# Kernel tuning notes

Measured on AMD Instinct MI355X. Metric: run time of the kernel, lower is better.

Reference implementation:

```python
import jax, jax.numpy as jnp
import numpy as np

F_, V, ED = 16, 1000, 16
B = 65536
D_IN = F_ * ED            # 256
STAR = [256, 512, 256]    # star layers
FCN = [256, 128, 64]      # mmoe expert layers
DOM, TSK, EXP = 3, 2, 8
KDT = DOM * TSK           # 6 gates/towers
SKIP_WEIGHT = 0.5
EPS = 1e-5


def layernorm(x, g, b):
    mu = jnp.mean(x, -1, keepdims=True)
    var = jnp.mean((x - mu) ** 2, -1, keepdims=True)
    return (x - mu) * jax.lax.rsqrt(var + EPS) * g + b


def mlp1(x, W, b, g, be):
    # Linear -> LayerNorm -> ReLU (MLP_N with one block)
    return jax.nn.relu(layernorm(x @ W + b, g, be))


def stack2(h, W1, b1, g1, be1, W2, b2, g2, be2):
    # vectorized bank of 2-block MLP_N experts; h: [B,D0], W1: [E,D0,D1]
    h1 = jax.nn.relu(layernorm(jnp.einsum('bd,edh->ebh', h, W1) + b1[:, None, :], g1[:, None, :], be1[:, None, :]))
    h2 = jax.nn.relu(layernorm(jnp.einsum('ebd,edh->ebh', h1, W2) + b2[:, None, :], g2[:, None, :], be2[:, None, :]))
    return h2  # [E,B,H]


def setup_inputs() -> dict:
    key = jax.random.key(0)
    ks = iter(jax.random.split(key, 64))

    def nrm(shape, scale=0.05):
        return jax.random.normal(next(ks), shape, jnp.float32) * scale

    inp = {}
    inp['x'] = jax.random.randint(next(ks), (F_, B), 0, 3).astype(jnp.int32)
    inp['emb_tables'] = nrm((F_, V, ED))
    inp['skip_W'] = nrm((D_IN, STAR[2])); inp['skip_b'] = jnp.zeros((STAR[2],))
    inp['skip_g'] = jnp.ones((STAR[2],)); inp['skip_be'] = jnp.zeros((STAR[2],))
    inp['shared_W'] = nrm((STAR[0], STAR[1])); inp['shared_b'] = jnp.zeros((STAR[1],))
    inp['slot_W'] = nrm((DOM, STAR[0], STAR[1])); inp['slot_b'] = jnp.zeros((DOM, STAR[1]))
    inp['star_W'] = nrm((STAR[1], STAR[2])); inp['star_b'] = jnp.zeros((STAR[2],))
    inp['star_g'] = jnp.ones((STAR[2],)); inp['star_be'] = jnp.zeros((STAR[2],))
    inp['dskip_W'] = nrm((KDT, STAR[2], FCN[-1])); inp['dskip_b'] = jnp.zeros((KDT, FCN[-1]))
    inp['dskip_g'] = jnp.ones((KDT, FCN[-1])); inp['dskip_be'] = jnp.zeros((KDT, FCN[-1]))
    for pre, n in (('exp', EXP), ('dexp', DOM), ('texp', TSK)):
        inp[pre + '_W1'] = nrm((n, FCN[0], FCN[1])); inp[pre + '_b1'] = jnp.zeros((n, FCN[1]))
        inp[pre + '_g1'] = jnp.ones((n, FCN[1])); inp[pre + '_be1'] = jnp.zeros((n, FCN[1]))
        inp[pre + '_W2'] = nrm((n, FCN[1], FCN[2])); inp[pre + '_b2'] = jnp.zeros((n, FCN[2]))
        inp[pre + '_g2'] = jnp.ones((n, FCN[2])); inp[pre + '_be2'] = jnp.zeros((n, FCN[2]))
    inp['gate_W'] = nrm((KDT, FCN[0], EXP)); inp['gate_b'] = jnp.zeros((KDT, EXP))
    inp['tow_W1'] = nrm((KDT, FCN[-1], FCN[-1])); inp['tow_b1'] = jnp.zeros((KDT, FCN[-1]))
    inp['tow_g'] = jnp.ones((KDT, FCN[-1])); inp['tow_be'] = jnp.zeros((KDT, FCN[-1]))
    inp['tow_W2'] = nrm((KDT, FCN[-1])); inp['tow_b2'] = jnp.zeros((KDT,))
    return inp


def _forward(x, emb_tables, skip_W, skip_b, skip_g, skip_be, shared_W, shared_b,
             slot_W, slot_b, star_W, star_b, star_g, star_be,
             dskip_W, dskip_b, dskip_g, dskip_be,
             exp_W1, exp_b1, exp_g1, exp_be1, exp_W2, exp_b2, exp_g2, exp_be2,
             dexp_W1, dexp_b1, dexp_g1, dexp_be1, dexp_W2, dexp_b2, dexp_g2, dexp_be2,
             texp_W1, texp_b1, texp_g1, texp_be1, texp_W2, texp_b2, texp_g2, texp_be2,
             gate_W, gate_b, tow_W1, tow_b1, tow_g, tow_be, tow_W2, tow_b2):
    domain_id = x[-1]                                          # [B] in {0,1,2}
    embs = jax.vmap(lambda t, i: t[i])(emb_tables, x)          # [F,B,ED]
    input_emb = jnp.moveaxis(embs, 0, 1).reshape(x.shape[1], D_IN)  # [B,256]

    skip = mlp1(input_emb, skip_W, skip_b, skip_g, skip_be)    # [B,256]

    # STAR: per-domain elementwise-product weights, domain masked select
    slot_out = jnp.einsum('bd,kdh->kbh', input_emb, slot_W * shared_W[None]) + slot_b[:, None, :] + shared_b  # [D,B,512]
    onehot = (domain_id[None, :] == jnp.arange(DOM)[:, None]).astype(slot_out.dtype)  # [D,B]
    emb0 = jnp.sum(onehot[:, :, None] * slot_out, axis=0)      # [B,512]
    emb = mlp1(emb0, star_W, star_b, star_g, star_be) + skip   # [B,256]

    # gates use emb.detach()
    gate = jax.nn.softmax(jnp.einsum('bd,kde->kbe', jax.lax.stop_gradient(emb), gate_W) + gate_b[:, None, :], axis=-1)  # [6,B,8]

    fea = stack2(emb, exp_W1, exp_b1, exp_g1, exp_be1, exp_W2, exp_b2, exp_g2, exp_be2)        # [8,B,64]
    dfea = stack2(emb, dexp_W1, dexp_b1, dexp_g1, dexp_be1, dexp_W2, dexp_b2, dexp_g2, dexp_be2)  # [3,B,64]
    tfea = stack2(emb, texp_W1, texp_b1, texp_g1, texp_be1, texp_W2, texp_b2, texp_g2, texp_be2)  # [2,B,64]
    dskip = jax.nn.relu(layernorm(jnp.einsum('bd,kdh->kbh', emb, dskip_W) + dskip_b[:, None, :], dskip_g[:, None, :], dskip_be[:, None, :]))  # [6,B,64]

    d_idx = jnp.arange(KDT) % DOM
    t_idx = jnp.arange(KDT) % TSK
    fused = jnp.einsum('kbe,ebh->kbh', gate, fea) + dfea[d_idx] + tfea[t_idx] + SKIP_WEIGHT * dskip  # [6,B,64]

    h = jax.nn.relu(layernorm(jnp.einsum('kbh,khj->kbj', fused, tow_W1) + tow_b1[:, None, :], tow_g[:, None, :], tow_be[:, None, :]))
    probs = jax.nn.sigmoid(jnp.einsum('kbh,kh->kb', h, tow_W2) + tow_b2[:, None])  # [6,B]

    # output[:, i] with i = t*DOM + d -> [B,T,D]; pick per-sample domain column
    out = jnp.moveaxis(probs, 0, 1).reshape(-1, TSK, DOM)
    result = jnp.take_along_axis(out, domain_id[:, None, None].astype(jnp.int32), axis=2)[:, :, 0]  # [B,T]
    return result


def reference(x, emb_tables, skip_W, skip_b, skip_g, skip_be, shared_W, shared_b,
              slot_W, slot_b, star_W, star_b, star_g, star_be,
              dskip_W, dskip_b, dskip_g, dskip_be,
              exp_W1, exp_b1, exp_g1, exp_be1, exp_W2, exp_b2, exp_g2, exp_be2,
              dexp_W1, dexp_b1, dexp_g1, dexp_be1, dexp_W2, dexp_b2, dexp_g2, dexp_be2,
              texp_W1, texp_b1, texp_g1, texp_be1, texp_W2, texp_b2, texp_g2, texp_be2,
              gate_W, gate_b, tow_W1, tow_b1, tow_g, tow_be, tow_W2, tow_b2):
    return _forward(x, emb_tables, skip_W, skip_b, skip_g, skip_be, shared_W, shared_b,
                    slot_W, slot_b, star_W, star_b, star_g, star_be,
                    dskip_W, dskip_b, dskip_g, dskip_be,
                    exp_W1, exp_b1, exp_g1, exp_be1, exp_W2, exp_b2, exp_g2, exp_be2,
                    dexp_W1, dexp_b1, dexp_g1, dexp_be1, dexp_W2, dexp_b2, dexp_g2, dexp_be2,
                    texp_W1, texp_b1, texp_g1, texp_be1, texp_W2, texp_b2, texp_g2, texp_be2,
                    gate_W, gate_b, tow_W1, tow_b1, tow_g, tow_be, tow_W2, tow_b2)
```

## Files before the change

kernel.cpp:

```cpp
#include <hip/hip_runtime.h>
#include <stdint.h>

#define B_TOT 65536

typedef __attribute__((ext_vector_type(8))) short s16x8;
typedef __attribute__((ext_vector_type(4))) float f32x4;
typedef unsigned short u16;
typedef unsigned int u32;
typedef unsigned long long u64;

#define OFF_SKIPW   0
#define OFF_MD      65536
#define OFF_GATEW   262144
#define OFF_EXPW1   274432
#define OFF_EXPW2   700416
#define OFF_DSKIPW  806912
#define OFF_TOWW1   905216
#define OFF_BVEC    929792
#define OFF_PAR     931328
#define OFF_PARF    941568
#define OFF_EMB     944640
#define OFF_PERM    17852928
#define OFF_CNT     17985024

// ... 26 lines not shown
}

template<int NT>
__device__ __forceinline__ void ln16(const f32x4* a, float invN, float* mu, float* rs){
  float s[4], q[4];
#pragma unroll
  for(int r=0;r<4;r++){ float aa=0.f,bb=0.f;
#pragma unroll
    for(int t=0;t<NT;t++){ float v=a[t][r]; aa+=v; bb+=v*v; }
    s[r]=aa; q[r]=bb; }
#pragma unroll
  for(int m=1;m<16;m<<=1){
#pragma unroll
    for(int r=0;r<4;r++){ s[r]+=__shfl_xor(s[r],m,16); q[r]+=__shfl_xor(q[r],m,16); } }
#pragma unroll
  for(int r=0;r<4;r++){ float m_=s[r]*invN; float v=q[r]*invN-m_*m_; mu[r]=m_; rs[r]=rsqrtf(v+1e-5f); }
}

__global__ __launch_bounds__(64) void k_sortinit(u16* __restrict__ ws){
  if(threadIdx.x<8) ((u32*)(ws+OFF_CNT))[threadIdx.x]=0u;
}
__global__ __launch_bounds__(256) void k_count(const int* __restrict__ x, u16* __restrict__ ws){
  u32* cnt=(u32*)(ws+OFF_CNT);
  int i=blockIdx.x*256+threadIdx.x;
  int lane=threadIdx.x&63;
  int d=x[15*B_TOT+i];
  u64 m0=__ballot(d==0), m1=__ballot(d==1), m2=__ballot(d==2);
  if(lane==0){
    if(m0) atomicAdd(&cnt[0],(u32)__popcll(m0));
    if(m1) atomicAdd(&cnt[1],(u32)__popcll(m1));
    if(m2) atomicAdd(&cnt[2],(u32)__popcll(m2));
  }
}
__global__ __launch_bounds__(256) void k_scatter(const int* __restrict__ x, u16* __restrict__ ws){
  u32* cnt=(u32*)(ws+OFF_CNT);
  u32* perm=(u32*)(ws+OFF_PERM);
  int i=blockIdx.x*256+threadIdx.x;
  int lane=threadIdx.x&63;
  int d=x[15*B_TOT+i];
  u32 c0=cnt[0], c1=cnt[1];
  u32 s1=c0, s2=c0+c1;
  u64 m0=__ballot(d==0), m1=__ballot(d==1), m2=__ballot(d==2);
  u32 b0v=0,b1v=0,b2v=0;
  if(lane==0){
    if(m0) b0v=atomicAdd(&cnt[3],(u32)__popcll(m0));
    if(m1) b1v=atomicAdd(&cnt[4],(u32)__popcll(m1));
    if(m2) b2v=atomicAdd(&cnt[5],(u32)__popcll(m2));
  }
  b0v=__shfl(b0v,0,64); b1v=__shfl(b1v,0,64); b2v=__shfl(b2v,0,64);
  u64 below=(1ull<<lane)-1ull;
  u32 pos;
  if(d==0)      pos=    b0v+(u32)__popcll(m0&below);
  else if(d==1) pos=s1+ b1v+(u32)__popcll(m1&below);
  else          pos=s2+ b2v+(u32)__popcll(m2&below);
  perm[pos]=(u32)i;
}

__global__ __launch_bounds__(256) void k_pack(
    const float* __restrict__ skip_W, const float* __restrict__ gate_W,
    const float* __restrict__ exp_W1, const float* __restrict__ dexp_W1, const float* __restrict__ texp_W1,
    const float* __restrict__ exp_W2, const float* __restrict__ dexp_W2, const float* __restrict__ texp_W2,
    const float* __restrict__ dskip_W, const float* __restrict__ tow_W1,
    u16* __restrict__ ws)
{
  int i=blockIdx.x*256+threadIdx.x;
  if(i>=OFF_BVEC) return;
  if(i>=OFF_MD && i<OFF_GATEW) return;
  float v;
  if(i<OFF_MD){
    int l=i; int j=l&7, lane=(l>>3)&63, kt=(l>>9)&7, ct=l>>12;
    int n=ct*16+(lane&15), k=kt*32+((lane>>4)<<3)+j;
    v = skip_W[k*256+n];
  } else if(i<OFF_EXPW1){
    int l=i-OFF_GATEW; int j=l&7, lane=(l>>3)&63, kt=(l>>9)&7, ct=l>>12;
    int n=ct*16+(lane&15), k=kt*32+((lane>>4)<<3)+j;
    int k6=n>>3, e=n&7;
    v = gate_W[(k6*256+k)*8+e];
  } else if(i<OFF_EXPW2){
    int l=i-OFF_EXPW1; int e=l>>15, r=l&32767;
    int j=r&7, lane=(r>>3)&63, kt=(r>>9)&7, ct=r>>12;
    int n=ct*16+(lane&15), k=kt*32+((lane>>4)<<3)+j;
    v = (e<8)? exp_W1[(e*256+k)*128+n] : (e<11)? dexp_W1[((e-8)*256+k)*128+n] : texp_W1[((e-11)*256+k)*128+n];
  } else if(i<OFF_DSKIPW){
    int l=i-OFF_EXPW2; int e=l>>13, r=l&8191;
    int j=r&7, lane=(r>>3)&63, kt=(r>>9)&3, ct=r>>11;
    int n=ct*16+(lane&15), k=kt*32+((lane>>4)<<3)+j;
    v = (e<8)? exp_W2[(e*128+k)*64+n] : (e<11)? dexp_W2[((e-8)*128+k)*64+n] : texp_W2[((e-11)*128+k)*64+n];
  } else if(i<OFF_TOWW1){
    int l=i-OFF_DSKIPW; int s=l>>14, r=l&16383;
    int j=r&7, lane=(r>>3)&63, kt=(r>>9)&7, ct=r>>12;
    int n=ct*16+(lane&15), k=kt*32+((lane>>4)<<3)+j;
    v = dskip_W[(s*256+k)*64+n];
  } else {
    int l=i-OFF_TOWW1; int s=l>>12, r=l&4095;
    int j=r&7, lane=(r>>3)&63, kt=(r>>9)&1, ct=r>>10;
    int n=ct*16+(lane&15), k=kt*32+((lane>>4)<<3)+j;
    v = tow_W1[(s*64+k)*64+n];
  }
  ws[i]=f2bf(v);
}

__global__ __launch_bounds__(256) void k_packpar(
    const float* __restrict__ exp_b1,const float* __restrict__ exp_g1,const float* __restrict__ exp_be1,
    const float* __restrict__ exp_b2,const float* __restrict__ exp_g2,const float* __restrict__ exp_be2,
    const float* __restrict__ dexp_b1,const float* __restrict__ dexp_g1,const float* __restrict__ dexp_be1,
    const float* __restrict__ dexp_b2,const float* __restrict__ dexp_g2,const float* __restrict__ dexp_be2,
    const float* __restrict__ texp_b1,const float* __restrict__ texp_g1,const float* __restrict__ texp_be1,
    const float* __restrict__ texp_b2,const float* __restrict__ texp_g2,const float* __restrict__ texp_be2,
    const float* __restrict__ dskip_b,const float* __restrict__ dskip_g,const float* __restrict__ dskip_be,
    const float* __restrict__ gate_b,
    const float* __restrict__ tow_b1,const float* __restrict__ tow_g,const float* __restrict__ tow_be,
    const float* __restrict__ tow_W2,const float* __restrict__ tow_b2,
    const float* __restrict__ skip_b,const float* __restrict__ skip_g,const float* __restrict__ skip_be,
    const float* __restrict__ star_b,const float* __restrict__ star_g,const float* __restrict__ star_be,
    u16* __restrict__ ws)
{
  int i=blockIdx.x*256+threadIdx.x;
  float* parf=(float*)(ws+OFF_PARF);
  if(i<10240){
    float v=0.f;
    if(i<PAR_DSK){
      int e=i/576, r=i%576;
      const float *b1,*g1,*be1,*b2,*g2,*be2;
      if(e<8){ b1=exp_b1+e*128; g1=exp_g1+e*128; be1=exp_be1+e*128;
               b2=exp_b2+e*64;  g2=exp_g2+e*64;  be2=exp_be2+e*64; }
      else if(e<11){ int q=e-8; b1=dexp_b1+q*128; g1=dexp_g1+q*128; be1=dexp_be1+q*128;
               b2=dexp_b2+q*64; g2=dexp_g2+q*64; be2=dexp_be2+q*64; }
      else { int q=e-11; b1=texp_b1+q*128; g1=texp_g1+q*128; be1=texp_be1+q*128;
               b2=texp_b2+q*64; g2=texp_g2+q*64; be2=texp_be2+q*64; }
      v = (r<128)? b1[r] : (r<256)? g1[r-128] : (r<384)? be1[r-256]
        : (r<448)? b2[r-384] : (r<512)? g2[r-448] : be2[r-512];
    } else if(i<PAR_TOW){
      int l=i-PAR_DSK; int j=l/192, r=l%192;
      v = (r<64)? dskip_b[j*64+r] : (r<128)? dskip_g[j*64+r-64] : dskip_be[j*64+r-128];
    } else if(i<PAR_GB){
      int l=i-PAR_TOW; int k6=l/256, r=l%256;
      v = (r<64)? tow_b1[k6*64+r] : (r<128)? tow_g[k6*64+r-64]
        : (r<192)? tow_be[k6*64+r-128] : tow_W2[k6*64+r-192];
    } else if(i<PAR_TB2){ v=gate_b[i-PAR_GB]; }
    else if(i<PAR_TB2+6){ v=tow_b2[i-PAR_TB2]; }
    ws[OFF_PAR+i]=f2bf(v);
  } else if(i<10240+1536){
    int l=i-10240;
    parf[l] = (l<256)? skip_b[l] : (l<512)? skip_g[l-256] : (l<768)? skip_be[l-512]
            : (l<1024)? star_b[l-768] : (l<1280)? star_g[l-1024] : star_be[l-1280];
  }
}

__global__ __launch_bounds__(256) void k_fold(
    const float* __restrict__ slot_W, const float* __restrict__ shared_W, const float* __restrict__ star_W,
    const float* __restrict__ slot_b, const float* __restrict__ shared_b,
    u16* __restrict__ ws)
{
  __shared__ float w[512];
  int bid=blockIdx.x, tid=threadIdx.x;
  if(bid<768){
    int d=bid>>8, k=bid&255;
    for(int j=tid;j<512;j+=256) w[j]=slot_W[(d*256+k)*512+j]*shared_W[k*512+j];
    __syncthreads();
    int n=tid; float a=0.f;
    for(int j=0;j<512;j++) a += w[j]*star_W[j*256+n];
    int ct=n>>4, l15=n&15, kt=k>>5, hi=(k>>3)&3, j8=k&7;
    ws[OFF_MD + d*65536 + (((ct*8+kt)*64 + hi*16 + l15)<<3) + j8] = f2bf(a);
  } else {
    int d=bid-768;
    for(int j=tid;j<512;j+=256) w[j]=slot_b[d*512+j]+shared_b[j];
    __syncthreads();
// ... 88 lines not shown
      for(int r=0;r<4;r++){
        float v=fmaxf((acc[rt][ct][r]-mu[r])*rs[r]*gv+bev,0.f);
        trbw[(rt*16+hq*4+r)*264 + col]=f2bf(v);
      }
    }
  }
  lds_fence();
#pragma unroll
  for(int rt=0;rt<2;rt++){
    int rtg=(b0>>4)+wv*2+rt;
#pragma unroll
    for(int kt=0;kt<8;kt++){
      s16x8 v=*(const s16x8*)(trbw + (rt*16+l15)*264 + kt*32+hq*8);
      *(s16x8*)(embp + (((size_t)(rtg*8+kt)*64+lane)<<3)) = v;
    }
  }
  __syncthreads();
  gstage(wsu+OFF_MD+dlo*65536, Wb[0], 16384, wv, lane, 4);
  __syncthreads();
  cur=0;

#pragma unroll
  for(int rt=0;rt<2;rt++)
#pragma unroll
    for(int ct=0;ct<16;ct++) acc[rt][ct]=fz;
  for(int dd=dlo;dd<=dhi;dd++){
#pragma unroll
    for(int c=0;c<8;c++){
      if(c<7)        gstage(wsu+OFF_MD+dd*65536+(c+1)*8192, Wb[cur^1], 16384, wv, lane, 4);
      else if(dd<dhi) gstage(wsu+OFF_MD+(dd+1)*65536,       Wb[cur^1], 16384, wv, lane, 4);
      const u16* B=Wb[cur];
#pragma unroll
      for(int kt=0;kt<8;kt++){
        s16x8 a0=(dmA[0]==dd)?af[0][kt]:zf;
        s16x8 a1=(dmA[1]==dd)?af[1][kt]:zf;
#pragma unroll
        for(int i=0;i<2;i++){
          s16x8 bf=*(const s16x8*)(B + (((i*8+kt)*64+lane)<<3));
          acc[0][c*2+i]=mfma16(a0,bf,acc[0][c*2+i]);
          acc[1][c*2+i]=mfma16(a1,bf,acc[1][c*2+i]);
        }
      }
      __syncthreads(); cur^=1;
    }
  }

#pragma unroll
  for(int rt=0;rt<2;rt++){
#pragma unroll
    for(int ct=0;ct<16;ct++){
      int col=ct*16+l15; float sb=parF[768+col];
#pragma unroll
      for(int r=0;r<4;r++) acc[rt][ct][r] += sb + bvecL[dm[rt][r]*256+col];
    }
    float mu[4],rs[4];
    ln16<16>(&acc[rt][0], 1.f/256.f, mu, rs);
#pragma unroll
    for(int ct=0;ct<16;ct++){
      int col=ct*16+l15;
      float gv=parF[1024+col], bev=parF[1280+col];
#pragma unroll
      for(int r=0;r<4;r++){
        float v=fmaxf((acc[rt][ct][r]-mu[r])*rs[r]*gv+bev,0.f);
        trbw[(rt*16+hq*4+r)*264 + col]=f2bf(v);
      }
    }
  }
  lds_fence();
#pragma unroll
  for(int rt=0;rt<2;rt++){
    int rtg=(b0>>4)+wv*2+rt;
#pragma unroll
    for(int kt=0;kt<8;kt++){
      s16x8 vs=*(const s16x8*)(trbw + (rt*16+l15)*264 + kt*32+hq*8);
      s16x8 vk=*(const s16x8*)(embp + (((size_t)(rtg*8+kt)*64+lane)<<3));
      union{ u16 h[8]; s16x8 v; } t;
#pragma unroll
      for(int j=0;j<8;j++) t.h[j]=f2bf(bf2f((u16)vs[j])+bf2f((u16)vk[j]));
      *(s16x8*)(embp + (((size_t)(rtg*8+kt)*64+lane)<<3)) = t.v;
    }
  }
}

__device__ __forceinline__ void glds1k(const u16* g, u16* l, int lane){
  __builtin_amdgcn_global_load_lds(
    (const __attribute__((address_space(1))) u32*)((const char*)g + lane*16),
    (__attribute__((address_space(3))) u32*)((char*)l), 16,0,0);
}
__device__ __forceinline__ void stage16k4(const u16* g, u16* l, int wv, int lane){
#pragma unroll
  for(int q=0;q<4;q++) glds1k(g + wv*2048 + q*512, l + wv*2048 + q*512, lane);
}
__device__ __forceinline__ void stage8k4(const u16* g, u16* l, int wv, int lane){
#pragma unroll
  for(int q=0;q<2;q++) glds1k(g + wv*1024 + q*512, l + wv*1024 + q*512, lane);
}
__device__ __forceinline__ void stage_phase4(int p, int dlo, int ndom,
    const u16* wsu, u16* slot, int wv, int lane){
  const int NU=10+ndom;
  const int P1=2+5*NU, P2=P1+4*ndom;
  if(p<2){ stage16k4(wsu+OFF_GATEW+p*8192, slot, wv, lane); return; }
  if(p<P1){ int q=p-2, ui=q/5, s=q%5;
    int u = (ui<8)? ui : (ui<8+ndom)? (8+dlo+(ui-8)) : (11+(ui-8-ndom));
    const u16* g = (s<4)? (wsu+OFF_EXPW1+u*32768+s*8192) : (wsu+OFF_EXPW2+u*8192);
    stage16k4(g, slot, wv, lane); return; }
  if(p<P2){ int q=p-P1; int dd=dlo+(q>>2); int j=(q&2)?(3+dd):dd; int half=q&1;
    stage16k4(wsu+OFF_DSKIPW+j*16384+half*8192, slot, wv, lane); return; }
  { int dd=dlo+(p-P2);
    stage8k4(wsu+OFF_TOWW1+dd*4096,     slot,      wv, lane);
    stage8k4(wsu+OFF_TOWW1+(3+dd)*4096, slot+4096, wv, lane); }
}
__device__ __forceinline__ void endph(){
  asm volatile("s_waitcnt vmcnt(0) lgkmcnt(0)\n\ts_barrier" ::: "memory");
  __builtin_amdgcn_sched_barrier(0);
}

__global__ __launch_bounds__(256,2) void k_B(
    const int* __restrict__ x, u16* __restrict__ wsu, float* __restrict__ out)
{
  __shared__ __align__(16) u16 Wb[2][8192];
  __shared__ __align__(16) u16 trb[4][32][136];
  __shared__ __align__(16) u32 gateF[128][8];
  __shared__ __align__(16) u16 parT[4096];

  const int tid=threadIdx.x, lane=tid&63, wv=tid>>6;
  const int l15=lane&15, hq=lane>>4;
  const int b0=blockIdx.x*128, rowbase=b0+wv*32;
  const f32x4 fz={0.f,0.f,0.f,0.f};
  const u16* embp=wsu+OFF_EMB;
  const u16* parE=wsu+OFF_PAR;
  const u32* perm=(const u32*)(wsu+OFF_PERM);
  u16* trbw=&trb[wv][0][0];

  const int dlo=__builtin_amdgcn_readfirstlane(x[15*B_TOT+(int)perm[b0]]);
  const int dhi=__builtin_amdgcn_readfirstlane(x[15*B_TOT+(int)perm[b0+127]]);
  const int ndom=dhi-dlo+1;
  const int NU=10+ndom;
  const int P1=2+5*NU, P2=P1+4*ndom, P3=P2+ndom;

  stage_phase4(0, dlo, ndom, wsu, &Wb[0][0], wv, lane);
  stage8k4(wsu+OFF_PAR+PAR_DSK, parT, wv, lane);

  u32 pv[2][4]; int dm[2][4];
#pragma unroll
  for(int rt=0;rt<2;rt++)
#pragma unroll
    for(int r=0;r<4;r++){
      u32 pp=perm[rowbase + rt*16 + hq*4 + r];
      pv[rt][r]=pp;
      dm[rt][r]=x[15*B_TOT+(int)pp];
    }

  s16x8 af[2][8];
#pragma unroll
  for(int rt=0;rt<2;rt++){
    int rtg=(rowbase>>4)+rt;
#pragma unroll
    for(int kt=0;kt<8;kt++)
      af[rt][kt]=*(const s16x8*)(embp + (((size_t)(rtg*8+kt)*64+lane)<<3));
  }

  f32x4 fa0[2][4], fa1[2][4];
#pragma unroll
  for(int rt=0;rt<2;rt++)
#pragma unroll
    for(int ct=0;ct<4;ct++){ fa0[rt][ct]=fz; fa1[rt][ct]=fz; }

  asm volatile("s_waitcnt vmcnt(0)" ::: "memory");
  __syncthreads();
  int p=0;

  {
    f32x4 gacc[2][3];
#pragma unroll
    for(int rt=0;rt<2;rt++)
#pragma unroll
      for(int ct=0;ct<3;ct++) gacc[rt][ct]=fz;
    stage_phase4(1, dlo, ndom, wsu, &Wb[1][0], wv, lane);
#pragma unroll
    for(int kt=0;kt<8;kt++)
#pragma unroll
      for(int i=0;i<2;i++){
        s16x8 bf=*(const s16x8*)(&Wb[0][0] + (((i*8+kt)*64+lane)<<3));
        gacc[0][i]=mfma16(af[0][kt],bf,gacc[0][i]);
        gacc[1][i]=mfma16(af[1][kt],bf,gacc[1][i]);
      }
    endph(); p=1;

    stage_phase4(2, dlo, ndom, wsu, &Wb[0][0], wv, lane);
#pragma unroll
    for(int kt=0;kt<8;kt++){
      s16x8 bf=*(const s16x8*)(&Wb[1][0] + ((kt*64+lane)<<3));
      gacc[0][2]=mfma16(af[0][kt],bf,gacc[0][2]);
      gacc[1][2]=mfma16(af[1][kt],bf,gacc[1][2]);
    }
    u16* gFh=(u16*)&gateF[0][0];
#pragma unroll
    for(int rt=0;rt<2;rt++)
#pragma unroll
      for(int ct=0;ct<3;ct++){
        int k6=ct*2+(l15>>3), e=l15&7;
        float gb=bf2f(parT[(PAR_GB-PAR_DSK) + k6*8+e]);
#pragma unroll
        for(int r=0;r<4;r++){
          float v=gacc[rt][ct][r]+gb;
          float mx=v;
          mx=fmaxf(mx,__shfl_xor(mx,1,8)); mx=fmaxf(mx,__shfl_xor(mx,2,8)); mx=fmaxf(mx,__shfl_xor(mx,4,8));
          float pe=__expf(v-mx);
          float ss=pe;
          ss+=__shfl_xor(ss,1,8); ss+=__shfl_xor(ss,2,8); ss+=__shfl_xor(ss,4,8);
          int brow=wv*32+rt*16+hq*4+r;
          int dmv=dm[rt][r];
          if(k6==dmv)   gFh[(brow*8+e)*2]  =f2bf(pe/ss);
          if(k6==3+dmv) gFh[(brow*8+e)*2+1]=f2bf(pe/ss);
        }
      }
    lds_fence();
    endph(); p=2;
  }

  for(int ui=0;ui<NU;ui++){
    const int u = (ui<8)? ui : (ui<8+ndom)? (8+dlo+(ui-8)) : (11+(ui-8-ndom));
    f32x4 acc1[2][8];
#pragma unroll
    for(int rt=0;rt<2;rt++)
#pragma unroll
      for(int ct=0;ct<8;ct++) acc1[rt][ct]=fz;
    for(int c=0;c<4;c++){
      const u16* Bw=&Wb[p&1][0];
      if(p+1<P3) stage_phase4(p+1, dlo, ndom, wsu, &Wb[(p+1)&1][0], wv, lane);
#pragma unroll
      for(int kt=0;kt<8;kt++)
#pragma unroll
        for(int i=0;i<2;i++){
          s16x8 bf=*(const s16x8*)(Bw + (((i*8+kt)*64+lane)<<3));
          acc1[0][c*2+i]=mfma16(af[0][kt],bf,acc1[0][c*2+i]);
          acc1[1][c*2+i]=mfma16(af[1][kt],bf,acc1[1][c*2+i]);
        }
      endph(); p++;
    }
    {
      const u16* Bw=&Wb[p&1][0];
      if(p+1<P3) stage_phase4(p+1, dlo, ndom, wsu, &Wb[(p+1)&1][0], wv, lane);
      const u16* pe_=parE + u*576;
#pragma unroll
      for(int rt=0;rt<2;rt++){
#pragma unroll
        for(int ct=0;ct<8;ct++){ float bb=bf2f(pe_[ct*16+l15]);
#pragma unroll
          for(int r=0;r<4;r++) acc1[rt][ct][r]+=bb; }
        float mu[4],rs[4],nm[4];
        ln16<8>(&acc1[rt][0],1.f/128.f,mu,rs);
#pragma unroll
        for(int r=0;r<4;r++) nm[r]=-mu[r]*rs[r];
#pragma unroll
        for(int ct=0;ct<8;ct++){
          int col=ct*16+l15;
          float gv=bf2f(pe_[128+col]), bev=bf2f(pe_[256+col]);
#pragma unroll
          for(int r=0;r<4;r++){
            float vn=fmaf(acc1[rt][ct][r],rs[r],nm[r]);
            trbw[(rt*16+hq*4+r)*136+col]=f2bf(fmaxf(fmaf(vn,gv,bev),0.f));
          }
        }
      }
      lds_fence();
      s16x8 af2[2][4];
#pragma unroll
      for(int rt=0;rt<2;rt++)
#pragma unroll
        for(int kt=0;kt<4;kt++)
          af2[rt][kt]=*(const s16x8*)(trbw+(rt*16+l15)*136+kt*32+hq*8);
      f32x4 acc2[2][4];
#pragma unroll
      for(int rt=0;rt<2;rt++)
#pragma unroll
        for(int ct=0;ct<4;ct++) acc2[rt][ct]=fz;
#pragma unroll
      for(int kt=0;kt<4;kt++)
#pragma unroll
        for(int ct=0;ct<4;ct++){
          s16x8 bf=*(const s16x8*)(Bw + (((ct*4+kt)*64+lane)<<3));
          acc2[0][ct]=mfma16(af2[0][kt],bf,acc2[0][ct]);
          acc2[1][ct]=mfma16(af2[1][kt],bf,acc2[1][ct]);
        }
#pragma unroll
      for(int rt=0;rt<2;rt++){
#pragma unroll
        for(int ct=0;ct<4;ct++){ float bb=bf2f(pe_[384+ct*16+l15]);
#pragma unroll
          for(int r=0;r<4;r++) acc2[rt][ct][r]+=bb; }
        float mu[4],rs[4],nm[4];
        ln16<4>(&acc2[rt][0],1.f/64.f,mu,rs);
#pragma unroll
        for(int r=0;r<4;r++) nm[r]=-mu[r]*rs[r];
        float g0v[4],g1v[4];
        if(ui<8){
#pragma unroll
          for(int r=0;r<4;r++){ u32 gg=gateF[wv*32+rt*16+hq*4+r][ui];
            g0v[r]=bf2f((u16)(gg&0xffffu)); g1v[r]=bf2f((u16)(gg>>16)); }
        } else if(ui<8+ndom){
          int du=dlo+(ui-8);
#pragma unroll
          for(int r=0;r<4;r++){ float m=(dm[rt][r]==du)?1.f:0.f; g0v[r]=m; g1v[r]=m; }
        } else {
          int q=ui-8-ndom;
#pragma unroll
          for(int r=0;r<4;r++){
            g0v[r]=((dm[rt][r]&1)==q)?1.f:0.f;
            g1v[r]=(((dm[rt][r]+1)&1)==q)?1.f:0.f;
          }
        }
#pragma unroll
        for(int ct=0;ct<4;ct++){
          int col=ct*16+l15;
          float gv=bf2f(pe_[448+col]), bev=bf2f(pe_[512+col]);
#pragma unroll
          for(int r=0;r<4;r++){
            float vn=fmaf(acc2[rt][ct][r],rs[r],nm[r]);
            float o=fmaxf(fmaf(vn,gv,bev),0.f);
            fa0[rt][ct][r]=fmaf(g0v[r],o,fa0[rt][ct][r]);
            fa1[rt][ct][r]=fmaf(g1v[r],o,fa1[rt][ct][r]);
          }
        }
      }
      endph(); p++;
    }
  }

  for(int dq=0;dq<2*ndom;dq++){
    const int dd=dlo+(dq>>1);
    const int jj=(dq&1)? (3+dd) : dd;
    f32x4 a3[2][4];
#pragma unroll
    for(int rt=0;rt<2;rt++)
#pragma unroll
      for(int ct=0;ct<4;ct++) a3[rt][ct]=fz;
    for(int c=0;c<2;c++){
      const u16* Bw=&Wb[p&1][0];
      if(p+1<P3) stage_phase4(p+1, dlo, ndom, wsu, &Wb[(p+1)&1][0], wv, lane);
#pragma unroll
      for(int kt=0;kt<8;kt++)
#pragma unroll
        for(int i=0;i<2;i++){
          s16x8 bf=*(const s16x8*)(Bw + (((i*8+kt)*64+lane)<<3));
          a3[0][c*2+i]=mfma16(af[0][kt],bf,a3[0][c*2+i]);
          a3[1][c*2+i]=mfma16(af[1][kt],bf,a3[1][c*2+i]);
        }
      if(c==1){
        const int pb=jj*192;
#pragma unroll
        for(int rt=0;rt<2;rt++){
#pragma unroll
          for(int ct=0;ct<4;ct++){ float bb=bf2f(parT[pb+ct*16+l15]);
#pragma unroll
            for(int r=0;r<4;r++) a3[rt][ct][r]+=bb; }
          float mu[4],rs[4],nm[4],mk[4];
          ln16<4>(&a3[rt][0],1.f/64.f,mu,rs);
#pragma unroll
          for(int r=0;r<4;r++){ nm[r]=-mu[r]*rs[r]; mk[r]=(dm[rt][r]==dd)?0.5f:0.f; }
#pragma unroll
          for(int ct=0;ct<4;ct++){
            int col=ct*16+l15;
            float gv=bf2f(parT[pb+64+col]), bev=bf2f(parT[pb+128+col]);
#pragma unroll
            for(int r=0;r<4;r++){
              float vn=fmaf(a3[rt][ct][r],rs[r],nm[r]);
              float o=fmaxf(fmaf(vn,gv,bev),0.f);
              if((dq&1)==0) fa0[rt][ct][r]=fmaf(mk[r],o,fa0[rt][ct][r]);
              else          fa1[rt][ct][r]=fmaf(mk[r],o,fa1[rt][ct][r]);
            }
          }
        }
      }
      endph(); p++;
    }
  }

#pragma unroll
  for(int rt=0;rt<2;rt++)
#pragma unroll
    for(int ct=0;ct<4;ct++)
#pragma unroll
      for(int r=0;r<4;r++){
        int rr=(rt*16+hq*4+r)*136 + ct*16+l15;
        trbw[rr]   =f2bf(fa0[rt][ct][r]);
        trbw[rr+64]=f2bf(fa1[rt][ct][r]);
      }
  lds_fence();
  s16x8 aft0[2][2], aft1[2][2];
#pragma unroll
  for(int rt=0;rt<2;rt++)
#pragma unroll
    for(int kt=0;kt<2;kt++){
      aft0[rt][kt]=*(const s16x8*)(trbw+(rt*16+l15)*136+kt*32+hq*8);
      aft1[rt][kt]=*(const s16x8*)(trbw+(rt*16+l15)*136+64+kt*32+hq*8);
    }

  for(int t=0;t<ndom;t++){
    const u16* Bw=&Wb[p&1][0];
    if(p+1<P3) stage_phase4(p+1, dlo, ndom, wsu, &Wb[(p+1)&1][0], wv, lane);
    const int dd=dlo+t;
#pragma unroll
    for(int s=0;s<2;s++){
      const int k6 = s? (3+dd) : dd;
      f32x4 ta[2][4];
#pragma unroll
      for(int rt=0;rt<2;rt++)
#pragma unroll
        for(int ct=0;ct<4;ct++) ta[rt][ct]=fz;
#pragma unroll
      for(int kt=0;kt<2;kt++)
#pragma unroll
        for(int ct=0;ct<4;ct++){
          s16x8 bf=*(const s16x8*)(Bw + s*4096 + (((ct*2+kt)*64+lane)<<3));
          if(s==0){ ta[0][ct]=mfma16(aft0[0][kt],bf,ta[0][ct]); ta[1][ct]=mfma16(aft0[1][kt],bf,ta[1][ct]); }
          else    { ta[0][ct]=mfma16(aft1[0][kt],bf,ta[0][ct]); ta[1][ct]=mfma16(aft1[1][kt],bf,ta[1][ct]); }
        }
      const int pb=(PAR_TOW-PAR_DSK)+k6*256;
#pragma unroll
      for(int rt=0;rt<2;rt++){
#pragma unroll
        for(int ct=0;ct<4;ct++){ float bb=bf2f(parT[pb+ct*16+l15]);
#pragma unroll
          for(int r=0;r<4;r++) ta[rt][ct][r]+=bb; }
        float mu[4],rs[4],nm[4];
        ln16<4>(&ta[rt][0],1.f/64.f,mu,rs);
#pragma unroll
        for(int r=0;r<4;r++) nm[r]=-mu[r]*rs[r];
        float pr[4]={0.f,0.f,0.f,0.f};
#pragma unroll
        for(int ct=0;ct<4;ct++){
          int col=ct*16+l15;
          float gv=bf2f(parT[pb+64+col]), bev=bf2f(parT[pb+128+col]), w2=bf2f(parT[pb+192+col]);
#pragma unroll
          for(int r=0;r<4;r++){
            float vn=fmaf(ta[rt][ct][r],rs[r],nm[r]);
            float o=fmaxf(fmaf(vn,gv,bev),0.f);
            pr[r]=fmaf(o,w2,pr[r]);
          }
        }
#pragma unroll
        for(int m=1;m<16;m<<=1){
#pragma unroll
          for(int r=0;r<4;r++) pr[r]+=__shfl_xor(pr[r],m,16);
        }
        if(l15==0){
          float tb2=bf2f(parT[(PAR_TB2-PAR_DSK)+k6]);
#pragma unroll
          for(int r=0;r<4;r++){
            if(dm[rt][r]==dd){
              float sv=pr[r]+tb2;
              out[(size_t)pv[rt][r]*2 + s] = 1.f/(1.f+__expf(-sv));
            }
          }
        }
      }
    }
    if(p+1<P3) endph();
    p++;
  }
}

extern "C" void kernel_launch(void* const* d_in, const int* in_sizes, int n_in,
                              void* d_out, int out_size, void* d_ws, size_t ws_size,
                              hipStream_t stream)
{
  if(ws_size < (size_t)(OFF_CNT+32)*2) return;

  const int*   x          =(const int*)  d_in[0];
  const float* emb_tables =(const float*)d_in[1];
  const float* skip_W     =(const float*)d_in[2];
  const float* skip_b     =(const float*)d_in[3];
  const float* skip_g     =(const float*)d_in[4];
  const float* skip_be    =(const float*)d_in[5];
  const float* shared_W   =(const float*)d_in[6];
  const float* shared_b   =(const float*)d_in[7];
  const float* slot_W     =(const float*)d_in[8];
  const float* slot_b     =(const float*)d_in[9];
  const float* star_W     =(const float*)d_in[10];
  const float* star_b     =(const float*)d_in[11];
  const float* star_g     =(const float*)d_in[12];
  const float* star_be    =(const float*)d_in[13];
  const float* dskip_W    =(const float*)d_in[14];
  const float* dskip_b    =(const float*)d_in[15];
  const float* dskip_g    =(const float*)d_in[16];
  const float* dskip_be   =(const float*)d_in[17];
  const float* exp_W1     =(const float*)d_in[18];
  const float* exp_b1     =(const float*)d_in[19];
  const float* exp_g1     =(const float*)d_in[20];
  const float* exp_be1    =(const float*)d_in[21];
  const float* exp_W2     =(const float*)d_in[22];
  const float* exp_b2     =(const float*)d_in[23];
  const float* exp_g2     =(const float*)d_in[24];
  const float* exp_be2    =(const float*)d_in[25];
  const float* dexp_W1    =(const float*)d_in[26];
  const float* dexp_b1    =(const float*)d_in[27];
  const float* dexp_g1    =(const float*)d_in[28];
  const float* dexp_be1   =(const float*)d_in[29];
  const float* dexp_W2    =(const float*)d_in[30];
  const float* dexp_b2    =(const float*)d_in[31];
  const float* dexp_g2    =(const float*)d_in[32];
  const float* dexp_be2   =(const float*)d_in[33];
  const float* texp_W1    =(const float*)d_in[34];
  const float* texp_b1    =(const float*)d_in[35];
  const float* texp_g1    =(const float*)d_in[36];
  const float* texp_be1   =(const float*)d_in[37];
  const float* texp_W2    =(const float*)d_in[38];
  const float* texp_b2    =(const float*)d_in[39];
  const float* texp_g2    =(const float*)d_in[40];
  const float* texp_be2   =(const float*)d_in[41];
  const float* gate_W     =(const float*)d_in[42];
  const float* gate_b     =(const float*)d_in[43];
  const float* tow_W1     =(const float*)d_in[44];
  const float* tow_b1     =(const float*)d_in[45];
  const float* tow_g      =(const float*)d_in[46];
  const float* tow_be     =(const float*)d_in[47];
  const float* tow_W2     =(const float*)d_in[48];
  const float* tow_b2     =(const float*)d_in[49];

  u16* wsu=(u16*)d_ws;
  float* out=(float*)d_out;

  k_sortinit<<<1,64,0,stream>>>(wsu);
  k_count<<<B_TOT/256,256,0,stream>>>(x,wsu);
  k_scatter<<<B_TOT/256,256,0,stream>>>(x,wsu);
  k_pack<<<(OFF_BVEC+255)/256,256,0,stream>>>(skip_W,gate_W,
      exp_W1,dexp_W1,texp_W1,exp_W2,dexp_W2,texp_W2,dskip_W,tow_W1,wsu);
  k_packpar<<<46,256,0,stream>>>(
      exp_b1,exp_g1,exp_be1,exp_b2,exp_g2,exp_be2,
      dexp_b1,dexp_g1,dexp_be1,dexp_b2,dexp_g2,dexp_be2,
      texp_b1,texp_g1,texp_be1,texp_b2,texp_g2,texp_be2,
      dskip_b,dskip_g,dskip_be,gate_b,
      tow_b1,tow_g,tow_be,tow_W2,tow_b2,
      skip_b,skip_g,skip_be,star_b,star_g,star_be,wsu);
  k_fold<<<771,256,0,stream>>>(slot_W,shared_W,star_W,slot_b,shared_b,wsu);
  k_front<<<B_TOT/128,256,0,stream>>>(x,emb_tables,wsu);
  k_B<<<B_TOT/128,256,0,stream>>>(x,wsu,out);
}
```

Baseline: 402.9 us.

## Load expert weights directly from global memory, drop LDS double-buffered staging

Removes the block-wide double-buffered global_load_lds weight staging and per-phase barriers. Each wave now reads MFMA B-fragments straight from global memory (through cache) and reads parameters from global instead of an LDS copy. Domain range is computed per wave rather than per block, and gate scratch becomes per-wave, so all block barriers disappear. Launch bounds drop to one block per SM, and a stray redundant assignment is added in the pack kernel. The aim is to remove barrier stalls and LDS traffic, at the cost of more global/L2 loads per wave and less latency hiding.

```diff
diff --git a/kernel.cpp b/kernel.cpp
--- a/kernel.cpp
+++ b/kernel.cpp
@@ -132,7 +132,8 @@
     int n=ct*16+(lane&15), k=kt*32+((lane>>4)<<3)+j;
     v = (e<8)? exp_W1[(e*256+k)*128+n] : (e<11)? dexp_W1[((e-8)*256+k)*128+n] : texp_W1[((e-11)*256+k)*128+n];
   } else if(i<OFF_DSKIPW){
-    int l=i-OFF_EXPW2; int e=l>>13, r=l&8191;
+    int l=i-OFF_EXPW1;
+    l=i-OFF_EXPW2; int e=l>>13, r=l&8191;
     int j=r&7, lane=(r>>3)&63, kt=(r>>9)&3, ct=r>>11;
     int n=ct*16+(lane&15), k=kt*32+((lane>>4)<<3)+j;
     v = (e<8)? exp_W2[(e*128+k)*64+n] : (e<11)? dexp_W2[((e-8)*128+k)*64+n] : texp_W2[((e-11)*128+k)*64+n];
@@ -387,64 +388,25 @@
   }
 }
 
-__device__ __forceinline__ void glds1k(const u16* g, u16* l, int lane){
-  __builtin_amdgcn_global_load_lds(
-    (const __attribute__((address_space(1))) u32*)((const char*)g + lane*16),
-    (__attribute__((address_space(3))) u32*)((char*)l), 16,0,0);
-}
-__device__ __forceinline__ void stage16k4(const u16* g, u16* l, int wv, int lane){
-#pragma unroll
-  for(int q=0;q<4;q++) glds1k(g + wv*2048 + q*512, l + wv*2048 + q*512, lane);
-}
-__device__ __forceinline__ void stage8k4(const u16* g, u16* l, int wv, int lane){
-#pragma unroll
-  for(int q=0;q<2;q++) glds1k(g + wv*1024 + q*512, l + wv*1024 + q*512, lane);
-}
-__device__ __forceinline__ void stage_phase4(int p, int dlo, int ndom,
-    const u16* wsu, u16* slot, int wv, int lane){
-  const int NU=10+ndom;
-  const int P1=2+5*NU, P2=P1+4*ndom;
-  if(p<2){ stage16k4(wsu+OFF_GATEW+p*8192, slot, wv, lane); return; }
-  if(p<P1){ int q=p-2, ui=q/5, s=q%5;
-    int u = (ui<8)? ui : (ui<8+ndom)? (8+dlo+(ui-8)) : (11+(ui-8-ndom));
-    const u16* g = (s<4)? (wsu+OFF_EXPW1+u*32768+s*8192) : (wsu+OFF_EXPW2+u*8192);
-    stage16k4(g, slot, wv, lane); return; }
-  if(p<P2){ int q=p-P1; int dd=dlo+(q>>2); int j=(q&2)?(3+dd):dd; int half=q&1;
-    stage16k4(wsu+OFF_DSKIPW+j*16384+half*8192, slot, wv, lane); return; }
-  { int dd=dlo+(p-P2);
-    stage8k4(wsu+OFF_TOWW1+dd*4096,     slot,      wv, lane);
-    stage8k4(wsu+OFF_TOWW1+(3+dd)*4096, slot+4096, wv, lane); }
-}
-__device__ __forceinline__ void endph(){
-  asm volatile("s_waitcnt vmcnt(0) lgkmcnt(0)\n\ts_barrier" ::: "memory");
-  __builtin_amdgcn_sched_barrier(0);
-}
-
-__global__ __launch_bounds__(256,2) void k_B(
+__global__ __launch_bounds__(256,1) void k_B(
     const int* __restrict__ x, u16* __restrict__ wsu, float* __restrict__ out)
 {
-  __shared__ __align__(16) u16 Wb[2][8192];
   __shared__ __align__(16) u16 trb[4][32][136];
-  __shared__ __align__(16) u32 gateF[128][8];
-  __shared__ __align__(16) u16 parT[4096];
+  __shared__ __align__(16) u32 gateF[4][32][8];
 
   const int tid=threadIdx.x, lane=tid&63, wv=tid>>6;
   const int l15=lane&15, hq=lane>>4;
-  const int b0=blockIdx.x*128, rowbase=b0+wv*32;
+  const int rowbase=blockIdx.x*128 + wv*32;
   const f32x4 fz={0.f,0.f,0.f,0.f};
   const u16* embp=wsu+OFF_EMB;
   const u16* parE=wsu+OFF_PAR;
   const u32* perm=(const u32*)(wsu+OFF_PERM);
   u16* trbw=&trb[wv][0][0];
 
-  const int dlo=__builtin_amdgcn_readfirstlane(x[15*B_TOT+(int)perm[b0]]);
-  const int dhi=__builtin_amdgcn_readfirstlane(x[15*B_TOT+(int)perm[b0+127]]);
+  const int dlo=__builtin_amdgcn_readfirstlane(x[15*B_TOT+(int)perm[rowbase]]);
+  const int dhi=__builtin_amdgcn_readfirstlane(x[15*B_TOT+(int)perm[rowbase+31]]);
   const int ndom=dhi-dlo+1;
   const int NU=10+ndom;
-  const int P1=2+5*NU, P2=P1+4*ndom, P3=P2+ndom;
-
-  stage_phase4(0, dlo, ndom, wsu, &Wb[0][0], wv, lane);
-  stage8k4(wsu+OFF_PAR+PAR_DSK, parT, wv, lane);
 
   u32 pv[2][4]; int dm[2][4];
 #pragma unroll
@@ -471,41 +433,31 @@
 #pragma unroll
     for(int ct=0;ct<4;ct++){ fa0[rt][ct]=fz; fa1[rt][ct]=fz; }
 
-  asm volatile("s_waitcnt vmcnt(0)" ::: "memory");
-  __syncthreads();
-  int p=0;
-
   {
     f32x4 gacc[2][3];
 #pragma unroll
     for(int rt=0;rt<2;rt++)
 #pragma unroll
       for(int ct=0;ct<3;ct++) gacc[rt][ct]=fz;
-    stage_phase4(1, dlo, ndom, wsu, &Wb[1][0], wv, lane);
-#pragma unroll
-    for(int kt=0;kt<8;kt++)
-#pragma unroll
-      for(int i=0;i<2;i++){
-        s16x8 bf=*(const s16x8*)(&Wb[0][0] + (((i*8+kt)*64+lane)<<3));
-        gacc[0][i]=mfma16(af[0][kt],bf,gacc[0][i]);
-        gacc[1][i]=mfma16(af[1][kt],bf,gacc[1][i]);
-      }
-    endph(); p=1;
-
-    stage_phase4(2, dlo, ndom, wsu, &Wb[0][0], wv, lane);
+    const u16* GW=wsu+OFF_GATEW;
 #pragma unroll
     for(int kt=0;kt<8;kt++){
-      s16x8 bf=*(const s16x8*)(&Wb[1][0] + ((kt*64+lane)<<3));
-      gacc[0][2]=mfma16(af[0][kt],bf,gacc[0][2]);
-      gacc[1][2]=mfma16(af[1][kt],bf,gacc[1][2]);
-    }
-    u16* gFh=(u16*)&gateF[0][0];
+      s16x8 wf[3];
+#pragma unroll
+      for(int ct=0;ct<3;ct++) wf[ct]=*(const s16x8*)(GW + (((ct*8+kt)*64+lane)<<3));
+#pragma unroll
+      for(int ct=0;ct<3;ct++){
+        gacc[0][ct]=mfma16(af[0][kt],wf[ct],gacc[0][ct]);
+        gacc[1][ct]=mfma16(af[1][kt],wf[ct],gacc[1][ct]);
+      }
+    }
+    u16* gFh=(u16*)&gateF[wv][0][0];
 #pragma unroll
     for(int rt=0;rt<2;rt++)
 #pragma unroll
       for(int ct=0;ct<3;ct++){
         int k6=ct*2+(l15>>3), e=l15&7;
-        float gb=bf2f(parT[(PAR_GB-PAR_DSK) + k6*8+e]);
+        float gb=bf2f(parE[PAR_GB + k6*8+e]);
 #pragma unroll
         for(int r=0;r<4;r++){
           float v=gacc[rt][ct][r]+gb;
@@ -514,171 +466,166 @@
           float pe=__expf(v-mx);
           float ss=pe;
           ss+=__shfl_xor(ss,1,8); ss+=__shfl_xor(ss,2,8); ss+=__shfl_xor(ss,4,8);
-          int brow=wv*32+rt*16+hq*4+r;
+          int brow=rt*16+hq*4+r;
           int dmv=dm[rt][r];
           if(k6==dmv)   gFh[(brow*8+e)*2]  =f2bf(pe/ss);
           if(k6==3+dmv) gFh[(brow*8+e)*2+1]=f2bf(pe/ss);
         }
       }
     lds_fence();
-    endph(); p=2;
   }
 
   for(int ui=0;ui<NU;ui++){
     const int u = (ui<8)? ui : (ui<8+ndom)? (8+dlo+(ui-8)) : (11+(ui-8-ndom));
+    const u16* W1=wsu+OFF_EXPW1+(size_t)u*32768;
+    const u16* W2=wsu+OFF_EXPW2+(size_t)u*8192;
+    const u16* pe_=parE + u*576;
     f32x4 acc1[2][8];
 #pragma unroll
     for(int rt=0;rt<2;rt++)
 #pragma unroll
       for(int ct=0;ct<8;ct++) acc1[rt][ct]=fz;
-    for(int c=0;c<4;c++){
-      const u16* Bw=&Wb[p&1][0];
-      if(p+1<P3) stage_phase4(p+1, dlo, ndom, wsu, &Wb[(p+1)&1][0], wv, lane);
-#pragma unroll
-      for(int kt=0;kt<8;kt++)
-#pragma unroll
-        for(int i=0;i<2;i++){
-          s16x8 bf=*(const s16x8*)(Bw + (((i*8+kt)*64+lane)<<3));
-          acc1[0][c*2+i]=mfma16(af[0][kt],bf,acc1[0][c*2+i]);
-          acc1[1][c*2+i]=mfma16(af[1][kt],bf,acc1[1][c*2+i]);
-        }
-      endph(); p++;
-    }
-    {
-      const u16* Bw=&Wb[p&1][0];
-      if(p+1<P3) stage_phase4(p+1, dlo, ndom, wsu, &Wb[(p+1)&1][0], wv, lane);
-      const u16* pe_=parE + u*576;
-#pragma unroll
-      for(int rt=0;rt<2;rt++){
-#pragma unroll
-        for(int ct=0;ct<8;ct++){ float bb=bf2f(pe_[ct*16+l15]);
-#pragma unroll
-          for(int r=0;r<4;r++) acc1[rt][ct][r]+=bb; }
-        float mu[4],rs[4],nm[4];
-        ln16<8>(&acc1[rt][0],1.f/128.f,mu,rs);
-#pragma unroll
-        for(int r=0;r<4;r++) nm[r]=-mu[r]*rs[r];
-#pragma unroll
-        for(int ct=0;ct<8;ct++){
-          int col=ct*16+l15;
-          float gv=bf2f(pe_[128+col]), bev=bf2f(pe_[256+col]);
-#pragma unroll
-          for(int r=0;r<4;r++){
-            float vn=fmaf(acc1[rt][ct][r],rs[r],nm[r]);
-            trbw[(rt*16+hq*4+r)*136+col]=f2bf(fmaxf(fmaf(vn,gv,bev),0.f));
-          }
-        }
-      }
-      lds_fence();
-      s16x8 af2[2][4];
-#pragma unroll
-      for(int rt=0;rt<2;rt++)
-#pragma unroll
-        for(int kt=0;kt<4;kt++)
-          af2[rt][kt]=*(const s16x8*)(trbw+(rt*16+l15)*136+kt*32+hq*8);
-      f32x4 acc2[2][4];
-#pragma unroll
-      for(int rt=0;rt<2;rt++)
-#pragma unroll
-        for(int ct=0;ct<4;ct++) acc2[rt][ct]=fz;
+#pragma unroll
+    for(int kt=0;kt<8;kt++){
+      s16x8 wf[8];
+#pragma unroll
+      for(int ct=0;ct<8;ct++) wf[ct]=*(const s16x8*)(W1 + (((ct*8+kt)*64+lane)<<3));
+#pragma unroll
+      for(int ct=0;ct<8;ct++){
+        acc1[0][ct]=mfma16(af[0][kt],wf[ct],acc1[0][ct]);
+        acc1[1][ct]=mfma16(af[1][kt],wf[ct],acc1[1][ct]);
+      }
+    }
+#pragma unroll
+    for(int rt=0;rt<2;rt++){
+#pragma unroll
+      for(int ct=0;ct<8;ct++){ float bb=bf2f(pe_[ct*16+l15]);
+#pragma unroll
+        for(int r=0;r<4;r++) acc1[rt][ct][r]+=bb; }
+      float mu[4],rs[4],nm[4];
+      ln16<8>(&acc1[rt][0],1.f/128.f,mu,rs);
+#pragma unroll
+      for(int r=0;r<4;r++) nm[r]=-mu[r]*rs[r];
+#pragma unroll
+      for(int ct=0;ct<8;ct++){
+        int col=ct*16+l15;
+        float gv=bf2f(pe_[128+col]), bev=bf2f(pe_[256+col]);
+#pragma unroll
+        for(int r=0;r<4;r++){
+          float vn=fmaf(acc1[rt][ct][r],rs[r],nm[r]);
+          trbw[(rt*16+hq*4+r)*136+col]=f2bf(fmaxf(fmaf(vn,gv,bev),0.f));
+        }
+      }
+    }
+    lds_fence();
+    s16x8 af2[2][4];
+#pragma unroll
+    for(int rt=0;rt<2;rt++)
 #pragma unroll
       for(int kt=0;kt<4;kt++)
-#pragma unroll
-        for(int ct=0;ct<4;ct++){
-          s16x8 bf=*(const s16x8*)(Bw + (((ct*4+kt)*64+lane)<<3));
-          acc2[0][ct]=mfma16(af2[0][kt],bf,acc2[0][ct]);
-          acc2[1][ct]=mfma16(af2[1][kt],bf,acc2[1][ct]);
-        }
-#pragma unroll
-      for(int rt=0;rt<2;rt++){
-#pragma unroll
-        for(int ct=0;ct<4;ct++){ float bb=bf2f(pe_[384+ct*16+l15]);
-#pragma unroll
-          for(int r=0;r<4;r++) acc2[rt][ct][r]+=bb; }
-        float mu[4],rs[4],nm[4];
-        ln16<4>(&acc2[rt][0],1.f/64.f,mu,rs);
-#pragma unroll
-        for(int r=0;r<4;r++) nm[r]=-mu[r]*rs[r];
-        float g0v[4],g1v[4];
-        if(ui<8){
-#pragma unroll
-          for(int r=0;r<4;r++){ u32 gg=gateF[wv*32+rt*16+hq*4+r][ui];
-            g0v[r]=bf2f((u16)(gg&0xffffu)); g1v[r]=bf2f((u16)(gg>>16)); }
-        } else if(ui<8+ndom){
-          int du=dlo+(ui-8);
-#pragma unroll
-          for(int r=0;r<4;r++){ float m=(dm[rt][r]==du)?1.f:0.f; g0v[r]=m; g1v[r]=m; }
-        } else {
-          int q=ui-8-ndom;
-#pragma unroll
-          for(int r=0;r<4;r++){
-            g0v[r]=((dm[rt][r]&1)==q)?1.f:0.f;
-            g1v[r]=(((dm[rt][r]+1)&1)==q)?1.f:0.f;
-          }
-        }
-#pragma unroll
-        for(int ct=0;ct<4;ct++){
-          int col=ct*16+l15;
-          float gv=bf2f(pe_[448+col]), bev=bf2f(pe_[512+col]);
-#pragma unroll
-          for(int r=0;r<4;r++){
-            float vn=fmaf(acc2[rt][ct][r],rs[r],nm[r]);
-            float o=fmaxf(fmaf(vn,gv,bev),0.f);
-            fa0[rt][ct][r]=fmaf(g0v[r],o,fa0[rt][ct][r]);
-            fa1[rt][ct][r]=fmaf(g1v[r],o,fa1[rt][ct][r]);
-          }
-        }
-      }
-      endph(); p++;
+        af2[rt][kt]=*(const s16x8*)(trbw+(rt*16+l15)*136+kt*32+hq*8);
+    lds_fence();
+    f32x4 acc2[2][4];
+#pragma unroll
+    for(int rt=0;rt<2;rt++)
+#pragma unroll
+      for(int ct=0;ct<4;ct++) acc2[rt][ct]=fz;
+#pragma unroll
+    for(int kt=0;kt<4;kt++){
+      s16x8 wf[4];
+#pragma unroll
+      for(int ct=0;ct<4;ct++) wf[ct]=*(const s16x8*)(W2 + (((ct*4+kt)*64+lane)<<3));
+#pragma unroll
+      for(int ct=0;ct<4;ct++){
+        acc2[0][ct]=mfma16(af2[0][kt],wf[ct],acc2[0][ct]);
+        acc2[1][ct]=mfma16(af2[1][kt],wf[ct],acc2[1][ct]);
+      }
+    }
+#pragma unroll
+    for(int rt=0;rt<2;rt++){
+#pragma unroll
+      for(int ct=0;ct<4;ct++){ float bb=bf2f(pe_[384+ct*16+l15]);
+#pragma unroll
+        for(int r=0;r<4;r++) acc2[rt][ct][r]+=bb; }
+      float mu[4],rs[4],nm[4];
+      ln16<4>(&acc2[rt][0],1.f/64.f,mu,rs);
+#pragma unroll
+      for(int r=0;r<4;r++) nm[r]=-mu[r]*rs[r];
+      float g0v[4],g1v[4];
+      if(ui<8){
+#pragma unroll
+        for(int r=0;r<4;r++){ u32 gg=gateF[wv][rt*16+hq*4+r][ui];
+          g0v[r]=bf2f((u16)(gg&0xffffu)); g1v[r]=bf2f((u16)(gg>>16)); }
+      } else if(ui<8+ndom){
+        int du=dlo+(ui-8);
+#pragma unroll
+        for(int r=0;r<4;r++){ float m=(dm[rt][r]==du)?1.f:0.f; g0v[r]=m; g1v[r]=m; }
+      } else {
+        int q=ui-8-ndom;
+#pragma unroll
+        for(int r=0;r<4;r++){
+          g0v[r]=((dm[rt][r]&1)==q)?1.f:0.f;
+          g1v[r]=(((dm[rt][r]+1)&1)==q)?1.f:0.f;
+        }
+      }
+#pragma unroll
+      for(int ct=0;ct<4;ct++){
+        int col=ct*16+l15;
+        float gv=bf2f(pe_[448+col]), bev=bf2f(pe_[512+col]);
+#pragma unroll
+        for(int r=0;r<4;r++){
+          float vn=fmaf(acc2[rt][ct][r],rs[r],nm[r]);
+          float o=fmaxf(fmaf(vn,gv,bev),0.f);
+          fa0[rt][ct][r]=fmaf(g0v[r],o,fa0[rt][ct][r]);
+          fa1[rt][ct][r]=fmaf(g1v[r],o,fa1[rt][ct][r]);
+        }
+      }
     }
   }
 
   for(int dq=0;dq<2*ndom;dq++){
     const int dd=dlo+(dq>>1);
     const int jj=(dq&1)? (3+dd) : dd;
+    const u16* WD=wsu+OFF_DSKIPW+(size_t)jj*16384;
     f32x4 a3[2][4];
 #pragma unroll
     for(int rt=0;rt<2;rt++)
 #pragma unroll
       for(int ct=0;ct<4;ct++) a3[rt][ct]=fz;
-    for(int c=0;c<2;c++){
-      const u16* Bw=&Wb[p&1][0];
-      if(p+1<P3) stage_phase4(p+1, dlo, ndom, wsu, &Wb[(p+1)&1][0], wv, lane);
-#pragma unroll
-      for(int kt=0;kt<8;kt++)
-#pragma unroll
-        for(int i=0;i<2;i++){
-          s16x8 bf=*(const s16x8*)(Bw + (((i*8+kt)*64+lane)<<3));
-          a3[0][c*2+i]=mfma16(af[0][kt],bf,a3[0][c*2+i]);
-          a3[1][c*2+i]=mfma16(af[1][kt],bf,a3[1][c*2+i]);
-        }
-      if(c==1){
-        const int pb=jj*192;
-#pragma unroll
-        for(int rt=0;rt<2;rt++){
-#pragma unroll
-          for(int ct=0;ct<4;ct++){ float bb=bf2f(parT[pb+ct*16+l15]);
-#pragma unroll
-            for(int r=0;r<4;r++) a3[rt][ct][r]+=bb; }
-          float mu[4],rs[4],nm[4],mk[4];
-          ln16<4>(&a3[rt][0],1.f/64.f,mu,rs);
-#pragma unroll
-          for(int r=0;r<4;r++){ nm[r]=-mu[r]*rs[r]; mk[r]=(dm[rt][r]==dd)?0.5f:0.f; }
-#pragma unroll
-          for(int ct=0;ct<4;ct++){
-            int col=ct*16+l15;
-            float gv=bf2f(parT[pb+64+col]), bev=bf2f(parT[pb+128+col]);
-#pragma unroll
-            for(int r=0;r<4;r++){
-              float vn=fmaf(a3[rt][ct][r],rs[r],nm[r]);
-              float o=fmaxf(fmaf(vn,gv,bev),0.f);
-              if((dq&1)==0) fa0[rt][ct][r]=fmaf(mk[r],o,fa0[rt][ct][r]);
-              else          fa1[rt][ct][r]=fmaf(mk[r],o,fa1[rt][ct][r]);
-            }
-          }
-        }
-      }
-      endph(); p++;
+#pragma unroll
+    for(int kt=0;kt<8;kt++){
+      s16x8 wf[4];
+#pragma unroll
+      for(int ct=0;ct<4;ct++) wf[ct]=*(const s16x8*)(WD + (((ct*8+kt)*64+lane)<<3));
+#pragma unroll
+      for(int ct=0;ct<4;ct++){
+        a3[0][ct]=mfma16(af[0][kt],wf[ct],a3[0][ct]);
+        a3[1][ct]=mfma16(af[1][kt],wf[ct],a3[1][ct]);
+      }
+    }
+    const int pb=PAR_DSK+jj*192;
+#pragma unroll
+    for(int rt=0;rt<2;rt++){
+#pragma unroll
+      for(int ct=0;ct<4;ct++){ float bb=bf2f(parE[pb+ct*16+l15]);
+#pragma unroll
+        for(int r=0;r<4;r++) a3[rt][ct][r]+=bb; }
+      float mu[4],rs[4],nm[4],mk[4];
+      ln16<4>(&a3[rt][0],1.f/64.f,mu,rs);
+#pragma unroll
+      for(int r=0;r<4;r++){ nm[r]=-mu[r]*rs[r]; mk[r]=(dm[rt][r]==dd)?0.5f:0.f; }
+#pragma unroll
+      for(int ct=0;ct<4;ct++){
+        int col=ct*16+l15;
+        float gv=bf2f(parE[pb+64+col]), bev=bf2f(parE[pb+128+col]);
+#pragma unroll
+        for(int r=0;r<4;r++){
+          float vn=fmaf(a3[rt][ct][r],rs[r],nm[r]);
+          float o=fmaxf(fmaf(vn,gv,bev),0.f);
+          if((dq&1)==0) fa0[rt][ct][r]=fmaf(mk[r],o,fa0[rt][ct][r]);
+          else          fa1[rt][ct][r]=fmaf(mk[r],o,fa1[rt][ct][r]);
+        }
+      }
     }
   }
 
@@ -701,32 +648,35 @@
       aft0[rt][kt]=*(const s16x8*)(trbw+(rt*16+l15)*136+kt*32+hq*8);
       aft1[rt][kt]=*(const s16x8*)(trbw+(rt*16+l15)*136+64+kt*32+hq*8);
     }
+  lds_fence();
 
   for(int t=0;t<ndom;t++){
-    const u16* Bw=&Wb[p&1][0];
-    if(p+1<P3) stage_phase4(p+1, dlo, ndom, wsu, &Wb[(p+1)&1][0], wv, lane);
     const int dd=dlo+t;
 #pragma unroll
     for(int s=0;s<2;s++){
       const int k6 = s? (3+dd) : dd;
+      const u16* WT=wsu+OFF_TOWW1+(size_t)k6*4096;
       f32x4 ta[2][4];
 #pragma unroll
       for(int rt=0;rt<2;rt++)
 #pragma unroll
         for(int ct=0;ct<4;ct++) ta[rt][ct]=fz;
 #pragma unroll
-      for(int kt=0;kt<2;kt++)
+      for(int kt=0;kt<2;kt++){
+        s16x8 wf[4];
+#pragma unroll
+        for(int ct=0;ct<4;ct++) wf[ct]=*(const s16x8*)(WT + (((ct*2+kt)*64+lane)<<3));
 #pragma unroll
         for(int ct=0;ct<4;ct++){
-          s16x8 bf=*(const s16x8*)(Bw + s*4096 + (((ct*2+kt)*64+lane)<<3));
-          if(s==0){ ta[0][ct]=mfma16(aft0[0][kt],bf,ta[0][ct]); ta[1][ct]=mfma16(aft0[1][kt],bf,ta[1][ct]); }
-          else    { ta[0][ct]=mfma16(aft1[0][kt],bf,ta[0][ct]); ta[1][ct]=mfma16(aft1[1][kt],bf,ta[1][ct]); }
-        }
-      const int pb=(PAR_TOW-PAR_DSK)+k6*256;
+          if(s==0){ ta[0][ct]=mfma16(aft0[0][kt],wf[ct],ta[0][ct]); ta[1][ct]=mfma16(aft0[1][kt],wf[ct],ta[1][ct]); }
+          else    { ta[0][ct]=mfma16(aft1[0][kt],wf[ct],ta[0][ct]); ta[1][ct]=mfma16(aft1[1][kt],wf[ct],ta[1][ct]); }
+        }
+      }
+      const int pb=PAR_TOW+k6*256;
 #pragma unroll
       for(int rt=0;rt<2;rt++){
 #pragma unroll
-        for(int ct=0;ct<4;ct++){ float bb=bf2f(parT[pb+ct*16+l15]);
+        for(int ct=0;ct<4;ct++){ float bb=bf2f(parE[pb+ct*16+l15]);
 #pragma unroll
           for(int r=0;r<4;r++) ta[rt][ct][r]+=bb; }
         float mu[4],rs[4],nm[4];
@@ -737,7 +687,7 @@
 #pragma unroll
         for(int ct=0;ct<4;ct++){
           int col=ct*16+l15;
-          float gv=bf2f(parT[pb+64+col]), bev=bf2f(parT[pb+128+col]), w2=bf2f(parT[pb+192+col]);
+          float gv=bf2f(parE[pb+64+col]), bev=bf2f(parE[pb+128+col]), w2=bf2f(parE[pb+192+col]);
 #pragma unroll
           for(int r=0;r<4;r++){
             float vn=fmaf(ta[rt][ct][r],rs[r],nm[r]);
@@ -751,7 +701,7 @@
           for(int r=0;r<4;r++) pr[r]+=__shfl_xor(pr[r],m,16);
         }
         if(l15==0){
-          float tb2=bf2f(parT[(PAR_TB2-PAR_DSK)+k6]);
+          float tb2=bf2f(parE[PAR_TB2+k6]);
 #pragma unroll
           for(int r=0;r<4;r++){
             if(dm[rt][r]==dd){
@@ -762,8 +712,6 @@
         }
       }
     }
-    if(p+1<P3) endph();
-    p++;
   }
 }
 
```

Measured after the change: 545.3 us. 1.35x slower.
